# Kernel tuning notes

Hardware: AMD Instinct MI355X
Metric: run time of the kernel (lower is better)

Reference implementation:

```python
import jax, jax.numpy as jnp
import numpy as np

B, S, H = 2, 2048, 1024
N_HEAD = 16
HEAD_DIM = H // N_HEAD


def setup_inputs() -> dict:
    key = jax.random.key(0)
    ks = jax.random.split(key, 8)
    init = 0.02
    return {
        "hidden_states": jax.random.normal(ks[0], (B, S, H), dtype=jnp.float32),
        "residual": jax.random.normal(ks[1], (B, S, H), dtype=jnp.float32),
        "alibi": jax.random.normal(ks[2], (B * N_HEAD, 1, S), dtype=jnp.float32),
        "attention_mask": jnp.ones((B, S), dtype=bool),
        "w_qkv": jax.random.normal(ks[3], (H, 3 * H), dtype=jnp.float32) * init,
        "b_qkv": jax.random.normal(ks[4], (3 * H,), dtype=jnp.float32) * init,
        "w_o": jax.random.normal(ks[5], (H, H), dtype=jnp.float32) * init,
        "b_o": jax.random.normal(ks[6], (H,), dtype=jnp.float32) * init,
        "layer_number": 4,
    }


def reference(hidden_states, residual, alibi, attention_mask, w_qkv, b_qkv, w_o, b_o, layer_number):
    b, s, h = hidden_states.shape
    nh, hd = N_HEAD, HEAD_DIM
    # fused QKV projection: (B,S,3H) -> (B,S,nh,3*hd) -> split
    fused_qkv = (hidden_states @ w_qkv + b_qkv).reshape(b, s, nh, 3 * hd)
    query, key, value = jnp.split(fused_qkv, 3, axis=-1)  # each (B,S,nh,hd)

    L = max(int(layer_number), 1)
    alpha = 1.0 / (np.sqrt(hd).astype(np.float32) * L)
    beta = 1.0 / L

    # scores = beta*alibi + alpha * q@k^T, reshaped to (B,nh,Sq,Sk)
    scores = jnp.einsum("bqnh,bknh->bnqk", query, key) * alpha
    scores = scores + beta * alibi.reshape(b, nh, 1, s)
    # FlaxBloomScaledSoftmax applies scale = layer_number before masking
    scores = scores * L

    # fused causal + padding mask (attention_mask_func): keep = causal & pad_q & pad_k
    causal = jnp.tril(jnp.ones((s, s), dtype=bool))
    pad = attention_mask  # (B,S) bool, True = attend
    keep = causal[None, None, :, :] & pad[:, None, :, None] & pad[:, None, None, :]  # (B,1,S,S)

    masked_scores = jnp.where(keep, scores, jnp.float32(-10000.0))
    probs = jax.nn.softmax(masked_scores.astype(jnp.float32), axis=-1) * keep
    probs = probs.astype(hidden_states.dtype)

    context = jnp.einsum("bnqk,bknh->bqnh", probs, value).reshape(b, s, h)
    attn_output = context @ w_o + b_o + residual
    return attn_output
```

## Files before the change

### kernel.cpp

```cpp
#include <hip/hip_runtime.h>
#include <hip/hip_bf16.h>

#define S_LEN 2048
#define HID   1024
#define NHEAD 16
#define HDIM  64
#define NBH   32

#define QSCALE 0.18033688f
#define LOG2E  1.44269504f

typedef __attribute__((ext_vector_type(8))) short short8;
typedef __attribute__((ext_vector_type(4))) float f32x4;

__device__ inline void gload_lds16(const void* g, void* l) {
  __builtin_amdgcn_global_load_lds(
      (const __attribute__((address_space(1))) void*)g,
      (__attribute__((address_space(3))) void*)l, 16, 0, 0);
}

__device__ inline ushort f2bf(float f) {
  __hip_bfloat16 h = __float2bfloat16(f);
  return *reinterpret_cast<const ushort*>(&h);
}

__device__ inline float exp2_fast(float x) {
  float r;
  asm("v_exp_f32 %0, %1" : "=v"(r) : "v"(x));
  return r;
}

__device__ inline void transpose_tile64(
    const float* __restrict__ in, ushort* __restrict__ out,
    int R, int C, int bx, int by, ushort (*Ls)[72])
{
    const int c0 = bx * 64, r0 = by * 64;
    const int t = threadIdx.x;
    const int tr = t >> 4, tc = (t & 15) * 4;
    #pragma unroll
    for (int i = 0; i < 4; ++i) {
        int gr = r0 + tr + i * 16;
        float4 v = *(const float4*)(in + (size_t)gr * C + c0 + tc);
        Ls[tc + 0][tr + i * 16] = f2bf(v.x);
        Ls[tc + 1][tr + i * 16] = f2bf(v.y);
        Ls[tc + 2][tr + i * 16] = f2bf(v.z);
        Ls[tc + 3][tr + i * 16] = f2bf(v.w);
    }
    __syncthreads();
    #pragma unroll
    for (int i = 0; i < 4; ++i) {
        int oc = c0 + tr + i * 16;
        ushort4 v = *(const ushort4*)&Ls[tr + i * 16][tc];
        *(ushort4*)(out + (size_t)oc * R + r0 + tc) = v;
    }
}

__global__ __launch_bounds__(256) void prep_fused(
    const float* __restrict__ X, ushort* __restrict__ Xb,
    const float* __restrict__ w_qkv, ushort* __restrict__ Wqkt,
    const float* __restrict__ w_o, ushort* __restrict__ Wot)
{
    __shared__ ushort Ls[64][72];
    const int b = blockIdx.x;
    if (b < 2048) {
        int i = b * 256 + threadIdx.x;
        float4 a = ((const float4*)X)[i * 2];
        float4 c = ((const float4*)X)[i * 2 + 1];
        union { ushort u[8]; uint4 v; } o;
        o.u[0]=f2bf(a.x); o.u[1]=f2bf(a.y); o.u[2]=f2bf(a.z); o.u[3]=f2bf(a.w);
        o.u[4]=f2bf(c.x); o.u[5]=f2bf(c.y); o.u[6]=f2bf(c.z); o.u[7]=f2bf(c.w);
        ((uint4*)Xb)[i] = o.v;
    } else if (b < 2816) {
        int t = b - 2048;
        transpose_tile64(w_qkv, Wqkt, 1024, 3072, t % 48, t / 48, Ls);
    } else {
        int t = b - 2816;
        transpose_tile64(w_o, Wot, 1024, 1024, t % 16, t / 16, Ls);
    }
}

__global__ __launch_bounds__(512, 2) void qkv_gemm_mfma(
    const ushort* __restrict__ A, const ushort* __restrict__ Bt,
    const float* __restrict__ bias,
    ushort* __restrict__ Q, ushort* __restrict__ K, ushort* __restrict__ V)
{
    __shared__ __align__(16) ushort smem[(2 * 256 + 2 * 192) * 64];
    ushort* const Asb = smem;
    ushort* const Bsb = smem + 2 * 256 * 64;
    const int tid = threadIdx.x;
    const int l   = tid & 63;
    const int w   = tid >> 6;
    const int wm  = w >> 2;
    const int wn  = w & 3;
    const int l7  = l & 7, l15 = l & 15, g = l >> 4;
    const int srow = l >> 3;
    const int schunk = l7 ^ srow;

    int lin = blockIdx.y * 16 + blockIdx.x;
    int swz = (lin & 7) * 32 + (lin >> 3);
    const int m0 = (swz >> 4) * 256;
    const int n0 = (swz & 15) * 192;

    f32x4 acc[8][3];
    #pragma unroll
    for (int i = 0; i < 8; ++i)
        #pragma unroll
        for (int j = 0; j < 3; ++j) acc[i][j] = (f32x4){0.f, 0.f, 0.f, 0.f};

#define STG_A(tt, qq) gload_lds16(A + (size_t)(m0 + (qq)*64 + w*8 + srow)*1024 \
                                    + (tt)*64 + schunk*8,                      \
                                  Asb + ((tt) & 1)*(256*64) + ((qq)*64 + w*8)*64)
#define STG_B(tt, qq) gload_lds16(Bt + (size_t)(n0 + (qq)*64 + w*8 + srow)*1024 \
                                    + (tt)*64 + schunk*8,                       \
                                  Bsb + ((tt) & 1)*(192*64) + ((qq)*64 + w*8)*64)
#define LD_A(bb, mf, kk) (*(const short8*)(Asb + (bb)*(256*64)                 \
                                           + ((mf)*32 + wm*16 + l15)*64        \
                                           + ((((kk)*4 + g) ^ l7) << 3)))
#define LD_B(bb, nf, kk) (*(const short8*)(Bsb + (bb)*(192*64)                 \
                                           + (wn*48 + (nf)*16 + l15)*64        \
                                           + ((((kk)*4 + g) ^ l7) << 3)))

    #pragma unroll
    for (int qq = 0; qq < 4; ++qq) STG_A(0, qq);
    #pragma unroll
    for (int qq = 0; qq < 3; ++qq) STG_B(0, qq);
    #pragma unroll
    for (int qq = 0; qq < 3; ++qq) { STG_A(1, qq); STG_B(1, qq); }
    asm volatile("s_waitcnt vmcnt(6)" ::: "memory");
    __builtin_amdgcn_s_barrier();

    short8 bfr[6];

    for (int it = 0; it < 8; ++it) {
        const int t = 2 * it;
        #pragma unroll
        for (int ph = 0; ph < 4; ++ph) {
            short8 afr[4];
            afr[0] = LD_A(0, 2*ph,     0);
            afr[1] = LD_A(0, 2*ph,     1);
            afr[2] = LD_A(0, 2*ph + 1, 0);
            afr[3] = LD_A(0, 2*ph + 1, 1);
            if (ph == 0) {
                #pragma unroll
                for (int nf = 0; nf < 3; ++nf) {
                    bfr[nf*2 + 0] = LD_B(0, nf, 0);
                    bfr[nf*2 + 1] = LD_B(0, nf, 1);
                }
            }
            if (ph == 0) { STG_A(t + 1, 3); }
            else if (t + 2 < 16) { STG_A(t + 2, ph - 1); STG_B(t + 2, ph - 1); }
            __builtin_amdgcn_s_barrier();
            asm volatile("s_waitcnt lgkmcnt(0)" ::: "memory");
            __builtin_amdgcn_sched_barrier(0);
            __builtin_amdgcn_s_setprio(1);
            #pragma unroll
            for (int kk = 0; kk < 2; ++kk)
                #pragma unroll
                for (int mi = 0; mi < 2; ++mi)
                    #pragma unroll
                    for (int nf = 0; nf < 3; ++nf)
                        acc[2*ph + mi][nf] = __builtin_amdgcn_mfma_f32_16x16x32_bf16(
                            afr[mi*2 + kk], bfr[nf*2 + kk], acc[2*ph + mi][nf], 0, 0, 0);
            __builtin_amdgcn_s_setprio(0);
            if (ph == 3) {
                if (it == 7) asm volatile("s_waitcnt vmcnt(0)" ::: "memory");
                else         asm volatile("s_waitcnt vmcnt(6)" ::: "memory");
            }
            __builtin_amdgcn_s_barrier();
        }
        #pragma unroll
        for (int ph = 0; ph < 4; ++ph) {
            short8 afr[4];
            afr[0] = LD_A(1, 2*ph,     0);
            afr[1] = LD_A(1, 2*ph,     1);
            afr[2] = LD_A(1, 2*ph + 1, 0);
            afr[3] = LD_A(1, 2*ph + 1, 1);
            if (ph == 0) {
                #pragma unroll
                for (int nf = 0; nf < 3; ++nf) {
                    bfr[nf*2 + 0] = LD_B(1, nf, 0);
                    bfr[nf*2 + 1] = LD_B(1, nf, 1);
                }
            }
            if (ph == 0) { if (t + 2 < 16) STG_A(t + 2, 3); }
            else if (t + 3 < 16) { STG_A(t + 3, ph - 1); STG_B(t + 3, ph - 1); }
            __builtin_amdgcn_s_barrier();
            asm volatile("s_waitcnt lgkmcnt(0)" ::: "memory");
            __builtin_amdgcn_sched_barrier(0);
            __builtin_amdgcn_s_setprio(1);
            #pragma unroll
            for (int kk = 0; kk < 2; ++kk)
                #pragma unroll
                for (int mi = 0; mi < 2; ++mi)
                    #pragma unroll
                    for (int nf = 0; nf < 3; ++nf)
                        acc[2*ph + mi][nf] = __builtin_amdgcn_mfma_f32_16x16x32_bf16(
                            afr[mi*2 + kk], bfr[nf*2 + kk], acc[2*ph + mi][nf], 0, 0, 0);
            __builtin_amdgcn_s_setprio(0);
            if (ph == 3) asm volatile("s_waitcnt vmcnt(6)" ::: "memory");
            __builtin_amdgcn_s_barrier();
        }
    }
#undef STG_A
#undef STG_B
#undef LD_A
#undef LD_B

    const int head = n0 / 192;
    ushort* const Cs = smem;
    #pragma unroll
    for (int nf = 0; nf < 3; ++nf) {
        int col = wn * 48 + nf * 16 + l15;
        float bv = bias[n0 + col];
        if (col >= 128) {
            int d = col - 128;
            #pragma unroll
            for (int mf = 0; mf < 8; ++mf) {
                int grow = m0 + mf * 32 + wm * 16 + g * 4;
                int bhh = ((grow >> 11) << 4) + head;
                int ss = grow & 2047;
                ushort4 pk;
                pk.x = f2bf(acc[mf][nf][0] + bv);
                pk.y = f2bf(acc[mf][nf][1] + bv);
                pk.z = f2bf(acc[mf][nf][2] + bv);
                pk.w = f2bf(acc[mf][nf][3] + bv);
                *(ushort4*)(V + ((size_t)bhh * 64 + d) * S_LEN + ss) = pk;
            }
        } else {
            float sc = (col < 64) ? QSCALE : 1.0f;
            #pragma unroll
            for (int mf = 0; mf < 8; ++mf) {
                int lr = mf * 32 + wm * 16 + g * 4;
                #pragma unroll
                for (int r = 0; r < 4; ++r)
                    Cs[(lr + r) * 132 + col] = f2bf((acc[mf][nf][r] + bv) * sc);
            }
        }
    }
    __syncthreads();
    {
        const int wq = w >> 2;
        ushort* const plane = wq ? K : Q;
        const int rbase = (w & 3) * 64;
        const int d = l15 * 4;
        #pragma unroll
        for (int i = 0; i < 16; ++i) {
            int lr = rbase + i * 4 + g;
            int grow = m0 + lr;
            int bhh = ((grow >> 11) << 4) + head;
            int ss = grow & 2047;
            ushort4 v = *(const ushort4*)&Cs[lr * 132 + wq * 64 + d];
            *(ushort4*)(plane + (((size_t)bhh * S_LEN + ss) << 6) + d) = v;
        }
    }
}

__global__ __launch_bounds__(512, 2) void out_gemm_mfma(
    const ushort* __restrict__ A, const ushort* __restrict__ Bt,
    const float* __restrict__ bias, const float* __restrict__ resid,
    float* __restrict__ out)
{
    __shared__ __align__(16) ushort As[2][256 * 64];
    __shared__ __align__(16) ushort Bs[2][64 * 64];
    const int tid = threadIdx.x;
    const int l   = tid & 63;
    const int w   = tid >> 6;
    const int wm  = w >> 2;
    const int wn  = w & 3;
    const int l7  = l & 7, l15 = l & 15, g = l >> 4;
    const int srow = l >> 3;
    const int schunk = l7 ^ srow;

    int lin = blockIdx.y * 16 + blockIdx.x;
    int swz = (lin & 7) * 32 + (lin >> 3);
    const int m0 = (swz >> 4) * 256;
    const int n0 = (swz & 15) * 64;

    f32x4 acc[8];
    #pragma unroll
    for (int i = 0; i < 8; ++i) acc[i] = (f32x4){0.f, 0.f, 0.f, 0.f};

#define OSTG_A(tt, qq) gload_lds16(A + (size_t)(m0 + (qq)*64 + w*8 + srow)*1024 \
                                     + (tt)*64 + schunk*8,                      \
                                   As[(tt) & 1] + ((qq)*64 + w*8)*64)
#define OSTG_B(tt)     gload_lds16(Bt + (size_t)(n0 + w*8 + srow)*1024          \
                                     + (tt)*64 + schunk*8,                      \
                                   Bs[(tt) & 1] + (w*8)*64)
#define OLD_A(bb, mf, kk) (*(const short8*)(As[bb] + ((mf)*32 + wm*16 + l15)*64 \
                                            + ((((kk)*4 + g) ^ l7) << 3)))
#define OLD_B(bb, kk)     (*(const short8*)(Bs[bb] + (wn*16 + l15)*64           \
                                            + ((((kk)*4 + g) ^ l7) << 3)))

    #pragma unroll
    for (int qq = 0; qq < 4; ++qq) OSTG_A(0, qq);
    OSTG_B(0);
    #pragma unroll
    for (int qq = 0; qq < 3; ++qq) OSTG_A(1, qq);
    OSTG_B(1);
    asm volatile("s_waitcnt vmcnt(4)" ::: "memory");
    __builtin_amdgcn_s_barrier();

    short8 bfr[2];

    for (int it = 0; it < 8; ++it) {
        const int t = 2 * it;
        #pragma unroll
        for (int ph = 0; ph < 4; ++ph) {
            short8 afr[4];
            afr[0] = OLD_A(0, 2*ph,     0);
            afr[1] = OLD_A(0, 2*ph,     1);
            afr[2] = OLD_A(0, 2*ph + 1, 0);
            afr[3] = OLD_A(0, 2*ph + 1, 1);
            if (ph == 0) { bfr[0] = OLD_B(0, 0); bfr[1] = OLD_B(0, 1); }
            if (ph == 0) { OSTG_A(t + 1, 3); }
            else if (t + 2 < 16) {
                OSTG_A(t + 2, ph - 1);
                if (ph == 1) OSTG_B(t + 2);
            }
            __builtin_amdgcn_s_barrier();
            asm volatile("s_waitcnt lgkmcnt(0)" ::: "memory");
            __builtin_amdgcn_sched_barrier(0);
            __builtin_amdgcn_s_setprio(1);
            #pragma unroll
            for (int kk = 0; kk < 2; ++kk)
                #pragma unroll
                for (int mi = 0; mi < 2; ++mi)
                    acc[2*ph + mi] = __builtin_amdgcn_mfma_f32_16x16x32_bf16(
                        afr[mi*2 + kk], bfr[kk], acc[2*ph + mi], 0, 0, 0);
            __builtin_amdgcn_s_setprio(0);
            if (ph == 3) {
                if (it == 7) asm volatile("s_waitcnt vmcnt(0)" ::: "memory");
                else         asm volatile("s_waitcnt vmcnt(4)" ::: "memory");
            }
            __builtin_amdgcn_s_barrier();
        }
        #pragma unroll
        for (int ph = 0; ph < 4; ++ph) {
            short8 afr[4];
            afr[0] = OLD_A(1, 2*ph,     0);
            afr[1] = OLD_A(1, 2*ph,     1);
            afr[2] = OLD_A(1, 2*ph + 1, 0);
            afr[3] = OLD_A(1, 2*ph + 1, 1);
            if (ph == 0) { bfr[0] = OLD_B(1, 0); bfr[1] = OLD_B(1, 1); }
            if (ph == 0) { if (t + 2 < 16) OSTG_A(t + 2, 3); }
            else if (t + 3 < 16) {
                OSTG_A(t + 3, ph - 1);
                if (ph == 1) OSTG_B(t + 3);
            }
            __builtin_amdgcn_s_barrier();
            asm volatile("s_waitcnt lgkmcnt(0)" ::: "memory");
            __builtin_amdgcn_sched_barrier(0);
            __builtin_amdgcn_s_setprio(1);
            #pragma unroll
            for (int kk = 0; kk < 2; ++kk)
                #pragma unroll
                for (int mi = 0; mi < 2; ++mi)
                    acc[2*ph + mi] = __builtin_amdgcn_mfma_f32_16x16x32_bf16(
                        afr[mi*2 + kk], bfr[kk], acc[2*ph + mi], 0, 0, 0);
            __builtin_amdgcn_s_setprio(0);
            if (ph == 3) asm volatile("s_waitcnt vmcnt(4)" ::: "memory");
            __builtin_amdgcn_s_barrier();
        }
    }
#undef OSTG_A
#undef OSTG_B
#undef OLD_A
#undef OLD_B

    {
        int gcol = n0 + wn * 16 + l15;
        float bv = bias[gcol];
        #pragma unroll
        for (int mf = 0; mf < 8; ++mf) {
            int grow = m0 + mf * 32 + wm * 16 + g * 4;
            #pragma unroll
            for (int r = 0; r < 4; ++r) {
                size_t idx = (size_t)(grow + r) * 1024 + gcol;
                out[idx] = acc[mf][r] + bv + resid[idx];
            }
        }
    }
}

#define STAGE(tt, idx) do {                                                   \
    gload_lds16(Kbh + (size_t)((tt) * 64 + w * 8 + srow) * 64 + schunk * 8,   \
                Ks[idx] + (w * 8) * 64);                                      \
    gload_lds16(Vbh + (size_t)(w * 8 + srow) * S_LEN + (tt) * 64 + schunk * 8,\
                Vs[idx] + (w * 8) * 64);                                      \
} while (0)

#define QK_TILE(SN, tt, idx, FULL) do {                                       \
    const ushort* Kc = Ks[idx];                                               \
    _Pragma("unroll")                                                         \
    for (int kb = 0; kb < 4; ++kb) {                                          \
        float4 a4 = *(const float4*)&alib[(tt) * 64 + kb * 16 + g * 4];       \
        SN[kb] = (f32x4){a4.x, a4.y, a4.z, a4.w};                             \
        if (FULL || (tt) * 64 + kb * 16 <= qmax) {                            \
            int row = kb * 16 + l15;                                          \
            short8 ka0 = *(const short8*)(Kc + row * 64 + ((g ^ l7) << 3));   \
            short8 ka1 = *(const short8*)(Kc + row * 64 + (((4+g) ^ l7) << 3));\
            SN[kb] = __builtin_amdgcn_mfma_f32_16x16x32_bf16(ka0, qb0, SN[kb], 0, 0, 0); \
            SN[kb] = __builtin_amdgcn_mfma_f32_16x16x32_bf16(ka1, qb1, SN[kb], 0, 0, 0); \
        }                                                                     \
    }                                                                         \
} while (0)

#define SM_PV(SC, tt, idx, FULL) do {                                         \
    const ushort* Vc = Vs[idx];                                               \
    ushort* Pw = Ps[w];                                                       \
    float p[16];                                                              \
    _Pragma("unroll")                                                         \
    for (int kb = 0; kb < 4; ++kb) {                                          \
        _Pragma("unroll")                                                     \
        for (int r = 0; r < 4; ++r) {                                         \
            float s = SC[kb][r];                                              \
            if (!FULL) {                                                      \
                int kglob = (tt) * 64 + kb * 16 + g * 4 + r;                  \
                s = (kglob > qglob) ? -1e30f : s;                             \
            }                                                                 \
            p[kb * 4 + r] = s;                                                \
        }                                                                     \
    }                                                                         \
    float mx0 = fmaxf(fmaxf(p[0], p[1]),   fmaxf(p[2], p[3]));                \
    float mx1 = fmaxf(fmaxf(p[4], p[5]),   fmaxf(p[6], p[7]));                \
    float mx2 = fmaxf(fmaxf(p[8], p[9]),   fmaxf(p[10], p[11]));              \
    float mx3 = fmaxf(fmaxf(p[12], p[13]), fmaxf(p[14], p[15]));              \
    float pmax = fmaxf(fmaxf(mx0, mx1), fmaxf(mx2, mx3));                     \
    pmax = fmaxf(pmax, __shfl_xor(pmax, 16));                                 \
    pmax = fmaxf(pmax, __shfl_xor(pmax, 32));                                 \
    if (!__all(pmax <= m + 11.5415603f)) {          \
        float mn = fmaxf(m, pmax);                                            \
        float resc = exp2_fast(m - mn);                                       \
        m = mn; lsum *= resc;                                                 \
        _Pragma("unroll")                                                     \
        for (int nb = 0; nb < 4; ++nb) oacc[nb] *= resc;                      \
    }                                                                         \
    _Pragma("unroll")                                                         \
    for (int i = 0; i < 16; ++i) p[i] = exp2_fast(p[i] - m);                  \
    float sm0 = (p[0] + p[1]) + (p[2] + p[3]);                                \
    float sm1 = (p[4] + p[5]) + (p[6] + p[7]);                                \
    float sm2 = (p[8] + p[9]) + (p[10] + p[11]);                              \
    float sm3 = (p[12] + p[13]) + (p[14] + p[15]);                            \
    float rsum = (sm0 + sm1) + (sm2 + sm3);                                   \
    rsum += __shfl_xor(rsum, 16);                                             \
    rsum += __shfl_xor(rsum, 32);                                             \
    lsum += rsum;                                                             \
    _Pragma("unroll")                                                         \
    for (int kb = 0; kb < 4; ++kb) {                                          \
        ushort4 pk;                                                           \
        pk.x = f2bf(p[kb * 4 + 0]); pk.y = f2bf(p[kb * 4 + 1]);               \
        pk.z = f2bf(p[kb * 4 + 2]); pk.w = f2bf(p[kb * 4 + 3]);               \
        int chunk = kb * 2 + (g >> 1);                                        \
        *(ushort4*)(Pw + l15 * 64 + ((chunk ^ l7) << 3) + ((g & 1) << 2)) = pk;\
    }                                                                         \
    short8 pb0 = *(const short8*)(Pw + l15 * 64 + ((g ^ l7) << 3));           \
    short8 pb1 = *(const short8*)(Pw + l15 * 64 + (((4 + g) ^ l7) << 3));     \
    _Pragma("unroll")                                                         \
    for (int nb = 0; nb < 4; ++nb) {                                          \
        int row = nb * 16 + l15;                                              \
        short8 va0 = *(const short8*)(Vc + row * 64 + ((g ^ l7) << 3));       \
        oacc[nb] = __builtin_amdgcn_mfma_f32_16x16x32_bf16(va0, pb0, oacc[nb], 0, 0, 0); \
    }                                                                         \
    if (FULL || (tt) * 64 + 32 <= qmax) {                                     \
        _Pragma("unroll")                                                     \
        for (int nb = 0; nb < 4; ++nb) {                                      \
            int row = nb * 16 + l15;                                          \
            short8 va1 = *(const short8*)(Vc + row * 64 + (((4 + g) ^ l7) << 3)); \
            oacc[nb] = __builtin_amdgcn_mfma_f32_16x16x32_bf16(va1, pb1, oacc[nb], 0, 0, 0); \
        }                                                                     \
    }                                                                         \
} while (0)

__global__ __launch_bounds__(512, 4) void attn_mfma(
    const ushort* __restrict__ Qp, const ushort* __restrict__ Kp,
    const ushort* __restrict__ Vtp, const float* __restrict__ alibi,
    ushort* __restrict__ ctx)
{
    __shared__ ushort Ks[3][64 * 64];
    __shared__ ushort Vs[3][64 * 64];
    __shared__ ushort Ps[8][16 * 64];
    __shared__ __align__(16) float alib[S_LEN];

    const int id  = blockIdx.x;
    const int bh  = id & 31;
    const int j   = id >> 5;
    const int qt  = (j < 8) ? (15 - j) : (j - 8);
    const int tid = threadIdx.x;
    const int w   = tid >> 6;
    const int l   = tid & 63;
    const int l7  = l & 7, l15 = l & 15, g = l >> 4;
    const int q0  = qt * 128;

    const ushort* Qbh = Qp  + (size_t)bh * S_LEN * HDIM;
    const ushort* Kbh = Kp  + (size_t)bh * S_LEN * HDIM;
    const ushort* Vbh = Vtp + (size_t)bh * HDIM * S_LEN;
    const float*  abh = alibi + (size_t)bh * S_LEN;

    const int qglob = q0 + w * 16 + l15;
    const int qmax  = q0 + w * 16 + 15;
    const int qmin  = q0 + w * 16;

    short8 qb0 = *(const short8*)(Qbh + (size_t)qglob * 64 + g * 8);
    short8 qb1 = *(const short8*)(Qbh + (size_t)qglob * 64 + 32 + g * 8);

    float m = -1e30f, lsum = 0.f;
    f32x4 oacc[4];
    #pragma unroll
    for (int nb = 0; nb < 4; ++nb) oacc[nb] = (f32x4){0.f, 0.f, 0.f, 0.f};

    const int srow   = l >> 3;
    const int schunk = (l & 7) ^ srow;

    {
        float4 a = *(const float4*)(abh + tid * 4);
        a.x *= LOG2E; a.y *= LOG2E; a.z *= LOG2E; a.w *= LOG2E;
        *(float4*)(alib + tid * 4) = a;
    }
    STAGE(0, 0);
    __syncthreads();
    STAGE(1, 1);

    f32x4 sa[4], sb[4];
    QK_TILE(sa, 0, 0, 0);

    const int nt = 2 * qt + 2;
    int ipv = 0, iqk = 1, ist = 2;
    for (int t = 0; t < nt; t += 2) {
        __syncthreads();
        if (t + 2 < nt) STAGE(t + 2, ist);
        if ((t + 1 < nt) && ((t + 1) * 64 + 63 <= qmin)) {
            QK_TILE(sb, t + 1, iqk, 1);
            SM_PV(sa, t, ipv, 1);
        } else {
            if ((t + 1 < nt) && ((t + 1) * 64 <= qmax)) QK_TILE(sb, t + 1, iqk, 0);
            if (t * 64 <= qmax) SM_PV(sa, t, ipv, 0);
        }
        { int tmp = ipv; ipv = iqk; iqk = ist; ist = tmp; }

        __syncthreads();
        if (t + 3 < nt) STAGE(t + 3, ist);
        if ((t + 2 < nt) && ((t + 2) * 64 + 63 <= qmin)) {
            QK_TILE(sa, t + 2, iqk, 1);
            SM_PV(sb, t + 1, ipv, 1);
        } else {
            if ((t + 2 < nt) && ((t + 2) * 64 <= qmax)) QK_TILE(sa, t + 2, iqk, 0);
            if ((t + 1) * 64 <= qmax) SM_PV(sb, t + 1, ipv, 0);
        }
        { int tmp = ipv; ipv = iqk; iqk = ist; ist = tmp; }
    }

    const int bb = bh >> 4, hh = bh & 15;
    float inv = 1.0f / lsum;
    ushort* crow = ctx + (size_t)(bb * S_LEN + qglob) * 1024 + hh * 64;
    #pragma unroll
    for (int nb = 0; nb < 4; ++nb) {
        ushort4 pk;
        pk.x = f2bf(oacc[nb][0] * inv);
        pk.y = f2bf(oacc[nb][1] * inv);
        pk.z = f2bf(oacc[nb][2] * inv);
        pk.w = f2bf(oacc[nb][3] * inv);
        *(ushort4*)(crow + nb * 16 + g * 4) = pk;
    }
}

extern "C" void kernel_launch(void* const* d_in, const int* in_sizes, int n_in,
                              void* d_out, int out_size, void* d_ws, size_t ws_size,
                              hipStream_t stream) {
    const float* X      = (const float*)d_in[0];
    const float* resid  = (const float*)d_in[1];
    const float* alibi  = (const float*)d_in[2];
    const float* w_qkv  = (const float*)d_in[4];
    const float* b_qkv  = (const float*)d_in[5];
    const float* w_o    = (const float*)d_in[6];
    const float* b_o    = (const float*)d_in[7];

    const size_t plane = (size_t)NBH * S_LEN * HDIM;
    ushort* Xb   = (ushort*)d_ws;
    ushort* Wqkt = Xb + (size_t)4096 * 1024;
    ushort* Wot  = Wqkt + (size_t)3072 * 1024;
    ushort* Qb   = Wot + (size_t)1024 * 1024;
    ushort* Kb   = Qb + plane;
    ushort* Vbt  = Qb + 2 * plane;
    ushort* ctx  = Qb + 3 * plane;
    float*  out  = (float*)d_out;

    prep_fused<<<3072, 256, 0, stream>>>(X, Xb, w_qkv, Wqkt, w_o, Wot);

    dim3 g1(3072 / 192, 4096 / 256);
    qkv_gemm_mfma<<<g1, 512, 0, stream>>>(Xb, Wqkt, b_qkv, Qb, Kb, Vbt);

    attn_mfma<<<512, 512, 0, stream>>>(Qb, Kb, Vbt, alibi, ctx);

    dim3 g3(1024 / 64, 4096 / 256);
    out_gemm_mfma<<<g3, 512, 0, stream>>>(ctx, Wot, b_o, resid, out);
}
```

Baseline: 108.8 us.

## Triple-buffer output GEMM LDS tiles and simplify per-k-step pipeline

Replaces the double-buffered, four-phase-per-tile staging in the output projection GEMM with a three-slot LDS ring. Each k-step loads all A and B fragments, issues the global-to-LDS prefetch for tile t+2, then runs 16 MFMAs, with only two barriers per tile instead of eight. The aim is to hide more global latency and cut synchronization overhead. In exchange, LDS use rises to about 120KB per block, which may cut occupancy below the two blocks per CU requested by launch bounds, and the fragment registers grow to 16 short8.

Measured after the change: 105.5 us (median of 2 runs). 1.03x faster.

```diff
diff --git a/kernel.cpp b/kernel.cpp
--- a/kernel.cpp
+++ b/kernel.cpp
@@ -260,8 +260,8 @@
     const float* __restrict__ bias, const float* __restrict__ resid,
     float* __restrict__ out)
 {
-    __shared__ __align__(16) ushort As[2][256 * 64];
-    __shared__ __align__(16) ushort Bs[2][64 * 64];
+    __shared__ __align__(16) ushort As3[3][256 * 64];
+    __shared__ __align__(16) ushort Bs3[3][64 * 64];
     const int tid = threadIdx.x;
     const int l   = tid & 63;
     const int w   = tid >> 6;
@@ -280,92 +280,58 @@
     #pragma unroll
     for (int i = 0; i < 8; ++i) acc[i] = (f32x4){0.f, 0.f, 0.f, 0.f};
 
-#define OSTG_A(tt, qq) gload_lds16(A + (size_t)(m0 + (qq)*64 + w*8 + srow)*1024 \
-                                     + (tt)*64 + schunk*8,                      \
-                                   As[(tt) & 1] + ((qq)*64 + w*8)*64)
-#define OSTG_B(tt)     gload_lds16(Bt + (size_t)(n0 + w*8 + srow)*1024          \
-                                     + (tt)*64 + schunk*8,                      \
-                                   Bs[(tt) & 1] + (w*8)*64)
-#define OLD_A(bb, mf, kk) (*(const short8*)(As[bb] + ((mf)*32 + wm*16 + l15)*64 \
-                                            + ((((kk)*4 + g) ^ l7) << 3)))
-#define OLD_B(bb, kk)     (*(const short8*)(Bs[bb] + (wn*16 + l15)*64           \
-                                            + ((((kk)*4 + g) ^ l7) << 3)))
-
-    #pragma unroll
-    for (int qq = 0; qq < 4; ++qq) OSTG_A(0, qq);
-    OSTG_B(0);
-    #pragma unroll
-    for (int qq = 0; qq < 3; ++qq) OSTG_A(1, qq);
-    OSTG_B(1);
-    asm volatile("s_waitcnt vmcnt(4)" ::: "memory");
+#define OSTG_A(tt, qq, bb) gload_lds16(                                        \
+        A + (size_t)(m0 + (qq)*64 + w*8 + srow)*1024 + (tt)*64 + schunk*8,     \
+        As3[bb] + ((qq)*64 + w*8)*64)
+#define OSTG_B(tt, bb)     gload_lds16(                                        \
+        Bt + (size_t)(n0 + w*8 + srow)*1024 + (tt)*64 + schunk*8,              \
+        Bs3[bb] + (w*8)*64)
+
+    #pragma unroll
+    for (int qq = 0; qq < 4; ++qq) OSTG_A(0, qq, 0);
+    OSTG_B(0, 0);
+    #pragma unroll
+    for (int qq = 0; qq < 4; ++qq) OSTG_A(1, qq, 1);
+    OSTG_B(1, 1);
+    asm volatile("s_waitcnt vmcnt(5)" ::: "memory");
     __builtin_amdgcn_s_barrier();
 
-    short8 bfr[2];
-
-    for (int it = 0; it < 8; ++it) {
-        const int t = 2 * it;
-        #pragma unroll
-        for (int ph = 0; ph < 4; ++ph) {
-            short8 afr[4];
-            afr[0] = OLD_A(0, 2*ph,     0);
-            afr[1] = OLD_A(0, 2*ph,     1);
-            afr[2] = OLD_A(0, 2*ph + 1, 0);
-            afr[3] = OLD_A(0, 2*ph + 1, 1);
-            if (ph == 0) { bfr[0] = OLD_B(0, 0); bfr[1] = OLD_B(0, 1); }
-            if (ph == 0) { OSTG_A(t + 1, 3); }
-            else if (t + 2 < 16) {
-                OSTG_A(t + 2, ph - 1);
-                if (ph == 1) OSTG_B(t + 2);
-            }
-            __builtin_amdgcn_s_barrier();
-            asm volatile("s_waitcnt lgkmcnt(0)" ::: "memory");
-            __builtin_amdgcn_sched_barrier(0);
-            __builtin_amdgcn_s_setprio(1);
+    int ir = 0, i1 = 1, is = 2;
+    for (int t = 0; t < 16; ++t) {
+        const ushort* Acur = As3[ir];
+        const ushort* Bcur = Bs3[ir];
+        short8 afr[16];
+        #pragma unroll
+        for (int mf = 0; mf < 8; ++mf)
             #pragma unroll
             for (int kk = 0; kk < 2; ++kk)
-                #pragma unroll
-                for (int mi = 0; mi < 2; ++mi)
-                    acc[2*ph + mi] = __builtin_amdgcn_mfma_f32_16x16x32_bf16(
-                        afr[mi*2 + kk], bfr[kk], acc[2*ph + mi], 0, 0, 0);
-            __builtin_amdgcn_s_setprio(0);
-            if (ph == 3) {
-                if (it == 7) asm volatile("s_waitcnt vmcnt(0)" ::: "memory");
-                else         asm volatile("s_waitcnt vmcnt(4)" ::: "memory");
-            }
-            __builtin_amdgcn_s_barrier();
-        }
-        #pragma unroll
-        for (int ph = 0; ph < 4; ++ph) {
-            short8 afr[4];
-            afr[0] = OLD_A(1, 2*ph,     0);
-            afr[1] = OLD_A(1, 2*ph,     1);
-            afr[2] = OLD_A(1, 2*ph + 1, 0);
-            afr[3] = OLD_A(1, 2*ph + 1, 1);
-            if (ph == 0) { bfr[0] = OLD_B(1, 0); bfr[1] = OLD_B(1, 1); }
-            if (ph == 0) { if (t + 2 < 16) OSTG_A(t + 2, 3); }
-            else if (t + 3 < 16) {
-                OSTG_A(t + 3, ph - 1);
-                if (ph == 1) OSTG_B(t + 3);
-            }
-            __builtin_amdgcn_s_barrier();
-            asm volatile("s_waitcnt lgkmcnt(0)" ::: "memory");
-            __builtin_amdgcn_sched_barrier(0);
-            __builtin_amdgcn_s_setprio(1);
-            #pragma unroll
-            for (int kk = 0; kk < 2; ++kk)
-                #pragma unroll
-                for (int mi = 0; mi < 2; ++mi)
-                    acc[2*ph + mi] = __builtin_amdgcn_mfma_f32_16x16x32_bf16(
-                        afr[mi*2 + kk], bfr[kk], acc[2*ph + mi], 0, 0, 0);
-            __builtin_amdgcn_s_setprio(0);
-            if (ph == 3) asm volatile("s_waitcnt vmcnt(4)" ::: "memory");
-            __builtin_amdgcn_s_barrier();
-        }
+                afr[mf*2 + kk] = *(const short8*)(
+                    Acur + (mf*32 + wm*16 + l15)*64 + ((((kk)*4 + g) ^ l7) << 3));
+        short8 bfr0 = *(const short8*)(Bcur + (wn*16 + l15)*64 + ((g ^ l7) << 3));
+        short8 bfr1 = *(const short8*)(Bcur + (wn*16 + l15)*64 + (((4 + g) ^ l7) << 3));
+        if (t + 2 < 16) {
+            #pragma unroll
+            for (int qq = 0; qq < 4; ++qq) OSTG_A(t + 2, qq, is);
+            OSTG_B(t + 2, is);
+        }
+        __builtin_amdgcn_s_barrier();
+        asm volatile("s_waitcnt lgkmcnt(0)" ::: "memory");
+        __builtin_amdgcn_sched_barrier(0);
+        __builtin_amdgcn_s_setprio(1);
+        #pragma unroll
+        for (int kk = 0; kk < 2; ++kk)
+            #pragma unroll
+            for (int mf = 0; mf < 8; ++mf)
+                acc[mf] = __builtin_amdgcn_mfma_f32_16x16x32_bf16(
+                    afr[mf*2 + kk], kk ? bfr1 : bfr0, acc[mf], 0, 0, 0);
+        __builtin_amdgcn_s_setprio(0);
+        if (t + 2 < 16) asm volatile("s_waitcnt vmcnt(5)" ::: "memory");
+        else            asm volatile("s_waitcnt vmcnt(0)" ::: "memory");
+        __builtin_amdgcn_s_barrier();
+        { int tmp = ir; ir = i1; i1 = is; is = tmp; }
     }
 #undef OSTG_A
 #undef OSTG_B
-#undef OLD_A
-#undef OLD_B
 
     {
         int gcol = n0 + wn * 16 + l15;
```
